# Performance work log

Hardware: AMD Instinct MI355X
Metric: run time of the kernel (lower is better)

The kernel has to match this reference:

```python
import jax, jax.numpy as jnp
import numpy as np

B, L, E, D = 4, 4096, 768, 64

def setup_inputs() -> dict:
    key = jax.random.key(0)
    ks = jax.random.split(key, 7)
    x = jax.random.normal(ks[0], (B, L, E), dtype=jnp.float32)
    # True = masked (strict upper triangle), as in masked_fill semantics
    causal_mask = jnp.triu(jnp.ones((L, L), dtype=bool), k=1)
    # True = valid token (inverted with ~ inside forward); all valid to avoid NaN rows
    pad_mask = jnp.ones((B, L), dtype=bool)
    s = 1.0 / np.sqrt(E)
    Wk = jax.random.uniform(ks[1], (E, D), jnp.float32, -s, s)
    bk = jax.random.uniform(ks[2], (D,), jnp.float32, -s, s)
    Wq = jax.random.uniform(ks[3], (E, D), jnp.float32, -s, s)
    bq = jax.random.uniform(ks[4], (D,), jnp.float32, -s, s)
    Wv = jax.random.uniform(ks[5], (E, D), jnp.float32, -s, s)
    bv = jax.random.uniform(ks[6], (D,), jnp.float32, -s, s)
    return {"x": x, "causal_mask": causal_mask, "pad_mask": pad_mask,
            "Wk": Wk, "bk": bk, "Wq": Wq, "bq": bq, "Wv": Wv, "bv": bv}

def reference(x, causal_mask, pad_mask, Wk, bk, Wq, bq, Wv, bv):
    # Linear projections: [B,L,E] @ [E,D] + [D]
    K = jnp.einsum('ble,ed->bld', x, Wk) + bk
    Q = jnp.einsum('ble,ed->bld', x, Wq) + bq
    V = jnp.einsum('ble,ed->bld', x, Wv) + bv
    d = Q.shape[-1]
    scores = jnp.einsum('bqd,bkd->bqk', Q, K) / jnp.sqrt(jnp.asarray(d, Q.dtype))
    # full_mask: causal (True=masked) OR key-position padding (~pad_mask, broadcast over query dim)
    full_mask = causal_mask[None, :, :] | (~pad_mask)[:, None, :]
    scores = jnp.where(full_mask, -jnp.inf, scores)
    attn = jax.nn.softmax(scores, axis=-1)
    out = jnp.einsum('bqk,bkd->bqd', attn, V)
    return out
```

## Files before the change

### kernel.cpp

```cpp
#include <hip/hip_runtime.h>

#define L_SEQ 4096
#define BATCH 4
#define EDIM 768

typedef __attribute__((ext_vector_type(8))) short bf16x8;
typedef __attribute__((ext_vector_type(4))) float f32x4;
typedef __attribute__((ext_vector_type(16))) float f32x16;
typedef __attribute__((ext_vector_type(4))) unsigned short u16x4;
typedef __attribute__((ext_vector_type(8))) unsigned short u16x8;
typedef __attribute__((ext_vector_type(2))) _Float16 f16x2;
typedef __attribute__((ext_vector_type(4))) _Float16 f16x4;

__device__ __forceinline__ unsigned short f2bf(float f) {
  unsigned u = __builtin_bit_cast(unsigned, f);
  u += 0x7FFFu + ((u >> 16) & 1u);
  return (unsigned short)(u >> 16);
}

__device__ __forceinline__ f16x4 half_of(u16x8 v, int h) {
  u16x4 t = h ? (u16x4){v[4], v[5], v[6], v[7]} : (u16x4){v[0], v[1], v[2], v[3]};
  return __builtin_bit_cast(f16x4, t);
}

__device__ __forceinline__ f16x2 pkrtz(float a, float b) {
  return __builtin_bit_cast(f16x2, __builtin_amdgcn_cvt_pkrtz(a, b));
}

__global__ __launch_bounds__(256) void prep_kernel(
    const float* __restrict__ Wq, const float* __restrict__ Wk,
    const float* __restrict__ Wv, unsigned short* __restrict__ WT) {
  int g = blockIdx.x * 256 + threadIdx.x;
  if (g >= 192 * EDIM) return;
  int row = g / EDIM, k = g - row * EDIM;
  int z = row >> 6, n = row & 63;
  const float* W = (z == 0) ? Wq : (z == 1) ? Wk : Wv;
  WT[g] = f2bf(W[k * 64 + n]);
}

__global__ __launch_bounds__(256) void proj_kernel(
    const float* __restrict__ x, const unsigned short* __restrict__ WT,
    const float* __restrict__ bq, const float* __restrict__ bk, const float* __restrict__ bv,
    unsigned short* __restrict__ Qf, unsigned short* __restrict__ Kf,
    unsigned short* __restrict__ Vf) {
  __shared__ unsigned short SH[2 * 13824];
  int tid = threadIdx.x;
  int w = tid >> 6, lane = tid & 63, l15 = lane & 15, g4 = lane >> 4;
  int m0 = blockIdx.x * 64;
  int brow = tid >> 3, bsg = tid & 7;

  f32x4 acc[3][4];
#pragma unroll
  for (int z = 0; z < 3; z++)
#pragma unroll
    for (int cf = 0; cf < 4; cf++) acc[z][cf] = (f32x4){0.f, 0.f, 0.f, 0.f};

  f32x4 arA[4], arB[4];
  u16x8 brA[6], brB[6];

  auto loadA = [&](f32x4 (&ar)[4], int k0) {
    const float* xp = x + (size_t)(m0 + 16 * w + l15) * EDIM + k0 + g4 * 8;
    ar[0] = *(const f32x4*)xp;
    ar[1] = *(const f32x4*)(xp + 4);
    ar[2] = *(const f32x4*)(xp + 32);
    ar[3] = *(const f32x4*)(xp + 36);
  };
  auto loadB = [&](u16x8 (&br)[6], int k0) {
#pragma unroll
    for (int pp = 0; pp < 6; pp++)
      br[pp] = *(const u16x8*)(WT + (size_t)(brow + pp * 32) * EDIM + k0 + bsg * 8);
  };
  auto writeB = [&](int cur, u16x8 (&br)[6]) {
#pragma unroll
    for (int pp = 0; pp < 6; pp++)
      *(u16x8*)&SH[cur * 13824 + (brow + pp * 32) * 72 + bsg * 8] = br[pp];
  };
  auto mkfrag = [&](f32x4 lo, f32x4 hi) {
    union { u16x8 u; bf16x8 b; } r;
    r.u[0] = f2bf(lo[0]); r.u[1] = f2bf(lo[1]); r.u[2] = f2bf(lo[2]); r.u[3] = f2bf(lo[3]);
    r.u[4] = f2bf(hi[0]); r.u[5] = f2bf(hi[1]); r.u[6] = f2bf(hi[2]); r.u[7] = f2bf(hi[3]);
    return r.b;
  };
  auto compute = [&](int cur, f32x4 (&ar)[4]) {
#pragma unroll
    for (int ks = 0; ks < 2; ks++) {
      bf16x8 a = mkfrag(ar[ks * 2], ar[ks * 2 + 1]);
#pragma unroll
      for (int z = 0; z < 3; z++)
#pragma unroll
        for (int cf = 0; cf < 4; cf++) {
          bf16x8 bb = *(const bf16x8*)&SH[cur * 13824 + (z * 64 + cf * 16 + l15) * 72 +
                                          ks * 32 + g4 * 8];
          acc[z][cf] = __builtin_amdgcn_mfma_f32_16x16x32_bf16(a, bb, acc[z][cf], 0, 0, 0);
        }
    }
  };

  loadA(arA, 0);
  loadB(brA, 0);
  for (int ss = 0; ss < 6; ss++) {
    int k1 = (2 * ss + 1) * 64;
    loadA(arB, k1);
    loadB(brB, k1);
    writeB(0, brA);
    __syncthreads();
    compute(0, arA);
    if (ss < 5) {
      int k2 = (2 * ss + 2) * 64;
      loadA(arA, k2);
      loadB(brA, k2);
    }
    writeB(1, brB);
    __syncthreads();
    compute(1, arB);
  }

  __syncthreads();
  unsigned short* LQ = SH;
  unsigned short* LK = SH + 4096;
  unsigned short* LV = SH + 8192;
#pragma unroll
  for (int cf = 0; cf < 4; cf++) {
    int d = cf * 16 + l15;
    float bqv = bq[d], bkv = bk[d], bvv = bv[d];
#pragma unroll
    for (int r = 0; r < 4; r++) {
      int t = 16 * w + g4 * 4 + r;
      int sl = t >> 5, tl = t & 31;
      int fqk = sl * 2048 + (d >> 4) * 512 + (tl + ((d >> 3) & 1) * 32) * 8 + (d & 7);
      LQ[fqk] = f2bf((acc[0][cf][r] + bqv) * 0.125f);
      LK[fqk] = f2bf(acc[1][cf][r] + bkv);
      int fv = sl * 2048 + (d >> 5) * 1024 + ((tl >> 4) & 1) * 512 +
               ((d & 31) + ((tl >> 2) & 1) * 32) * 8 + ((tl >> 3) & 1) * 4 + (tl & 3);
      _Float16 hv = (_Float16)(acc[2][cf][r] + bvv);
      LV[fv] = __builtin_bit_cast(unsigned short, hv);
    }
  }
  __syncthreads();
  {
    int bb = m0 >> 12;
    int S0 = (m0 >> 5) & 127;
    size_t base = ((size_t)(bb * 128 + S0)) * 2048;
    u16x8* dq = (u16x8*)(Qf + base);
    u16x8* dk = (u16x8*)(Kf + base);
    u16x8* dv = (u16x8*)(Vf + base);
    const u16x8* sq = (const u16x8*)LQ;
    const u16x8* sk = (const u16x8*)LK;
    const u16x8* sv = (const u16x8*)LV;
    dq[tid * 2] = sq[tid * 2]; dq[tid * 2 + 1] = sq[tid * 2 + 1];
    dk[tid * 2] = sk[tid * 2]; dk[tid * 2 + 1] = sk[tid * 2 + 1];
    dv[tid * 2] = sv[tid * 2]; dv[tid * 2 + 1] = sv[tid * 2 + 1];
  }
}

__global__ __launch_bounds__(512, 2) void attn_kernel(
    const unsigned short* __restrict__ Qf, const unsigned short* __restrict__ Kf,
    const unsigned short* __restrict__ Vf, float* __restrict__ out) {
  __shared__ float OB[8][32][68];
  __shared__ float ML[8][2][32];
  int tid = threadIdx.x;
  int w = tid >> 6, lane = tid & 63;
  int ql = lane & 31, hi = lane >> 5;
  int blk = blockIdx.x;
  int xcd = blk & 7;
  int b = xcd >> 1;
  int pid = ((xcd & 1) << 5) | (blk >> 3);
  int sA = pid, sB = 127 - pid;
  size_t bL = (size_t)b * L_SEQ;
  const unsigned short* Qb = Qf + (size_t)b * 128 * 2048;
  const unsigned short* Kb = Kf + (size_t)b * 128 * 2048;
  const unsigned short* Vb = Vf + (size_t)b * 128 * 2048;

  bf16x8 qA[4], qB[4];
#pragma unroll
  for (int kh = 0; kh < 4; kh++) {
    qA[kh] = *(const bf16x8*)(Qb + ((size_t)sA * 4 + kh) * 512 + lane * 8);
    qB[kh] = *(const bf16x8*)(Qb + ((size_t)sB * 4 + kh) * 512 + lane * 8);
  }
  f32x16 oA0, oA1, oB0, oB1;
#pragma unroll
  for (int i = 0; i < 16; i++) { oA0[i] = 0.f; oA1[i] = 0.f; oB0[i] = 0.f; oB1[i] = 0.f; }
  float mA = -1e38f, lA = 0.f, mB = -1e38f, lB = 0.f;

  auto loadKV = [&](bf16x8 (&kf)[4], u16x8 (&vf)[4], int j) {
    const unsigned short* kp = Kb + (size_t)j * 2048 + lane * 8;
    const unsigned short* vp = Vb + (size_t)j * 2048 + lane * 8;
#pragma unroll
    for (int q = 0; q < 4; q++) kf[q] = *(const bf16x8*)(kp + q * 512);
#pragma unroll
    for (int q = 0; q < 4; q++) vf[q] = *(const u16x8*)(vp + q * 512);
  };

  auto strip = [&](bf16x8 (&kf)[4], u16x8 (&vf)[4], int j, int s, bf16x8 (&qf)[4],
                   f32x16& o0, f32x16& o1, float& m, float& l) {
    f32x16 st;
#pragma unroll
    for (int i = 0; i < 16; i++) st[i] = 0.f;
    __builtin_amdgcn_s_setprio(1);
#pragma unroll
    for (int kh = 0; kh < 4; kh++)
      st = __builtin_amdgcn_mfma_f32_32x32x16_bf16(kf[kh], qf[kh], st, 0, 0, 0);
    __builtin_amdgcn_s_setprio(0);

    if (j == s) {
#pragma unroll
      for (int r = 0; r < 16; r++) {
        int tl = (r & 3) + 8 * (r >> 2) + 4 * hi;
        if (tl > ql) st[r] = -1e30f;
      }
    }

    float mx = st[0];
#pragma unroll
    for (int r = 1; r < 16; r++) mx = fmaxf(mx, st[r]);
    mx = fmaxf(mx, __shfl_xor(mx, 32));
    if (!__all(mx <= m + 8.0f)) {
      float mn = fmaxf(m, mx);
      float sc = __expf(m - mn);
      m = mn; l *= sc;
#pragma unroll
      for (int i = 0; i < 16; i++) { o0[i] *= sc; o1[i] *= sc; }
    }
    float rs = 0.f;
#pragma unroll
    for (int r = 0; r < 16; r++) { st[r] = __expf(st[r] - m); rs += st[r]; }
    rs += __shfl_xor(rs, 32);
    l += rs;

    f16x4 pb[4];
#pragma unroll
    for (int oc = 0; oc < 4; oc++) {
      f16x2 a = pkrtz(st[4 * oc], st[4 * oc + 1]);
      f16x2 c = pkrtz(st[4 * oc + 2], st[4 * oc + 3]);
      pb[oc] = (f16x4){a[0], a[1], c[0], c[1]};
    }
    __builtin_amdgcn_s_setprio(1);
#pragma unroll
    for (int oc = 0; oc < 4; oc++)
      o0 = __builtin_amdgcn_mfma_f32_32x32x8f16(half_of(vf[oc >> 1], oc & 1), pb[oc], o0, 0, 0, 0);
#pragma unroll
    for (int oc = 0; oc < 4; oc++)
      o1 = __builtin_amdgcn_mfma_f32_32x32x8f16(half_of(vf[2 + (oc >> 1)], oc & 1), pb[oc], o1, 0, 0, 0);
    __builtin_amdgcn_s_setprio(0);
  };

  auto step = [&](bf16x8 (&kf)[4], u16x8 (&vf)[4], int j) {
    if (j <= sA) strip(kf, vf, j, sA, qA, oA0, oA1, mA, lA);
    strip(kf, vf, j, sB, qB, oB0, oB1, mB, lB);
  };

  bf16x8 kfA[4], kfB[4];
  u16x8 vfA[4], vfB[4];
  {
    int j = w;
    loadKV(kfA, vfA, j);
    while (true) {
      int jn = j + 8;
      bool hasB = (jn <= sB);
      if (hasB) loadKV(kfB, vfB, jn);
      step(kfA, vfA, j);
      if (!hasB) break;
      j = jn;
      jn = j + 8;
      bool hasA = (jn <= sB);
      if (hasA) loadKV(kfA, vfA, jn);
      step(kfB, vfB, j);
      if (!hasA) break;
      j = jn;
    }
  }

  auto stash_reduce = [&](int s, f32x16& o0, f32x16& o1, float m, float l) {
    __syncthreads();
#pragma unroll
    for (int g = 0; g < 4; g++) {
      *(f32x4*)&OB[w][ql][8 * g + 4 * hi] =
          (f32x4){o0[4 * g], o0[4 * g + 1], o0[4 * g + 2], o0[4 * g + 3]};
      *(f32x4*)&OB[w][ql][32 + 8 * g + 4 * hi] =
          (f32x4){o1[4 * g], o1[4 * g + 1], o1[4 * g + 2], o1[4 * g + 3]};
    }
    if (hi == 0) { ML[w][0][ql] = m; ML[w][1][ql] = l; }
    __syncthreads();
    int q = tid >> 4, dg = tid & 15;
    float mw[8], lw[8];
    float ms = -1e38f;
#pragma unroll
    for (int ww = 0; ww < 8; ww++) {
      mw[ww] = ML[ww][0][q]; lw[ww] = ML[ww][1][q];
      ms = fmaxf(ms, mw[ww]);
    }
    float denom = 0.f, ew[8];
#pragma unroll
    for (int ww = 0; ww < 8; ww++) { ew[ww] = __expf(mw[ww] - ms); denom += lw[ww] * ew[ww]; }
    float inv = 1.0f / denom;
    f32x4 acc = (f32x4){0.f, 0.f, 0.f, 0.f};
#pragma unroll
    for (int ww = 0; ww < 8; ww++) {
      f32x4 v = *(const f32x4*)&OB[ww][q][dg * 4];
      acc += v * ew[ww];
    }
    acc *= inv;
    *(f32x4*)(out + (bL + (size_t)s * 32 + q) * 64 + dg * 4) = acc;
  };
  stash_reduce(sA, oA0, oA1, mA, lA);
  stash_reduce(sB, oB0, oB1, mB, lB);
}

extern "C" void kernel_launch(void* const* d_in, const int* in_sizes, int n_in,
                              void* d_out, int out_size, void* d_ws, size_t ws_size,
                              hipStream_t stream) {
  const float* x  = (const float*)d_in[0];
  const float* Wk = (const float*)d_in[3];
  const float* bk = (const float*)d_in[4];
  const float* Wq = (const float*)d_in[5];
  const float* bq = (const float*)d_in[6];
  const float* Wv = (const float*)d_in[7];
  const float* bv = (const float*)d_in[8];
  float* out = (float*)d_out;

  char* ws = (char*)d_ws;
  unsigned short* WT = (unsigned short*)ws;
  unsigned short* Qf = (unsigned short*)(ws + 294912);
  unsigned short* Kf = (unsigned short*)(ws + 294912 + 2097152);
  unsigned short* Vf = (unsigned short*)(ws + 294912 + 2 * 2097152);

  prep_kernel<<<576, 256, 0, stream>>>(Wq, Wk, Wv, WT);
  proj_kernel<<<256, 256, 0, stream>>>(x, WT, bq, bk, bv, Qf, Kf, Vf);
  attn_kernel<<<256, 512, 0, stream>>>(Qf, Kf, Vf, out);
}
```

Baseline: 48.13 us.

## Stage projection weights directly into LDS with pre-swizzled layout via global_load_lds

The weight-transpose prep kernel now writes the bf16 weights in a per-k-step tiled layout with an XOR swizzle. The projection kernel then copies each tile straight from global memory into LDS using global_load_lds, with no register round trip. The LDS tile drops its padding and the reads apply the matching XOR swizzle to avoid bank conflicts. The pipeline is reordered so each stage issues its loads before computing on the other buffer, which cuts VGPR pressure and copy instructions. This relies on correct ordering between the async LDS loads and the barriers.

```diff
diff --git a/kernel.cpp b/kernel.cpp
--- a/kernel.cpp
+++ b/kernel.cpp
@@ -27,27 +27,35 @@
   return __builtin_bit_cast(f16x2, __builtin_amdgcn_cvt_pkrtz(a, b));
 }
 
+__device__ __forceinline__ void gload_lds16(const void* g, void* l) {
+  __builtin_amdgcn_global_load_lds(
+      (const __attribute__((address_space(1))) void*)g,
+      (__attribute__((address_space(3))) void*)l, 16, 0, 0);
+}
+
 __global__ __launch_bounds__(256) void prep_kernel(
     const float* __restrict__ Wq, const float* __restrict__ Wk,
-    const float* __restrict__ Wv, unsigned short* __restrict__ WT) {
+    const float* __restrict__ Wv, unsigned short* __restrict__ WTT) {
   int g = blockIdx.x * 256 + threadIdx.x;
-  if (g >= 192 * EDIM) return;
-  int row = g / EDIM, k = g - row * EDIM;
+  int kstep = g / 12288, rem = g - kstep * 12288;
+  int row = rem >> 6, kc_lin = rem & 63;
   int z = row >> 6, n = row & 63;
+  int kc = kc_lin ^ ((row & 7) << 3);
+  int k = kstep * 64 + kc;
   const float* W = (z == 0) ? Wq : (z == 1) ? Wk : Wv;
-  WT[g] = f2bf(W[k * 64 + n]);
+  WTT[g] = f2bf(W[k * 64 + n]);
 }
 
 __global__ __launch_bounds__(256) void proj_kernel(
-    const float* __restrict__ x, const unsigned short* __restrict__ WT,
+    const float* __restrict__ x, const unsigned short* __restrict__ WTT,
     const float* __restrict__ bq, const float* __restrict__ bk, const float* __restrict__ bv,
     unsigned short* __restrict__ Qf, unsigned short* __restrict__ Kf,
     unsigned short* __restrict__ Vf) {
-  __shared__ unsigned short SH[2 * 13824];
+  __shared__ unsigned short SH[2 * 12288];
   int tid = threadIdx.x;
   int w = tid >> 6, lane = tid & 63, l15 = lane & 15, g4 = lane >> 4;
   int m0 = blockIdx.x * 64;
-  int brow = tid >> 3, bsg = tid & 7;
+  int sw = (l15 & 7) << 3;
 
   f32x4 acc[3][4];
 #pragma unroll
@@ -56,7 +64,6 @@
     for (int cf = 0; cf < 4; cf++) acc[z][cf] = (f32x4){0.f, 0.f, 0.f, 0.f};
 
   f32x4 arA[4], arB[4];
-  u16x8 brA[6], brB[6];
 
   auto loadA = [&](f32x4 (&ar)[4], int k0) {
     const float* xp = x + (size_t)(m0 + 16 * w + l15) * EDIM + k0 + g4 * 8;
@@ -65,15 +72,13 @@
     ar[2] = *(const f32x4*)(xp + 32);
     ar[3] = *(const f32x4*)(xp + 36);
   };
-  auto loadB = [&](u16x8 (&br)[6], int k0) {
-#pragma unroll
-    for (int pp = 0; pp < 6; pp++)
-      br[pp] = *(const u16x8*)(WT + (size_t)(brow + pp * 32) * EDIM + k0 + bsg * 8);
-  };
-  auto writeB = [&](int cur, u16x8 (&br)[6]) {
-#pragma unroll
-    for (int pp = 0; pp < 6; pp++)
-      *(u16x8*)&SH[cur * 13824 + (brow + pp * 32) * 72 + bsg * 8] = br[pp];
+  auto stageB = [&](int buf, int kstep) {
+    const unsigned short* src = WTT + (size_t)kstep * 12288;
+#pragma unroll
+    for (int i = 0; i < 6; i++) {
+      int c = i * 4 + w;
+      gload_lds16(src + c * 512 + lane * 8, &SH[buf * 12288 + c * 512]);
+    }
   };
   auto mkfrag = [&](f32x4 lo, f32x4 hi) {
     union { u16x8 u; bf16x8 b; } r;
@@ -89,33 +94,30 @@
       for (int z = 0; z < 3; z++)
 #pragma unroll
         for (int cf = 0; cf < 4; cf++) {
-          bf16x8 bb = *(const bf16x8*)&SH[cur * 13824 + (z * 64 + cf * 16 + l15) * 72 +
-                                          ks * 32 + g4 * 8];
+          bf16x8 bb = *(const bf16x8*)&SH[cur * 12288 + (z * 64 + cf * 16 + l15) * 64 +
+                                          ((ks * 32 + g4 * 8) ^ sw)];
           acc[z][cf] = __builtin_amdgcn_mfma_f32_16x16x32_bf16(a, bb, acc[z][cf], 0, 0, 0);
         }
     }
   };
 
+  stageB(0, 0);
   loadA(arA, 0);
-  loadB(brA, 0);
+  __syncthreads();
   for (int ss = 0; ss < 6; ss++) {
-    int k1 = (2 * ss + 1) * 64;
-    loadA(arB, k1);
-    loadB(brB, k1);
-    writeB(0, brA);
+    int t1 = 2 * ss + 1;
+    stageB(1, t1);
+    loadA(arB, t1 * 64);
+    compute(0, arA);
     __syncthreads();
-    compute(0, arA);
     if (ss < 5) {
-      int k2 = (2 * ss + 2) * 64;
-      loadA(arA, k2);
-      loadB(brA, k2);
-    }
-    writeB(1, brB);
+      stageB(0, t1 + 1);
+      loadA(arA, (t1 + 1) * 64);
+    }
+    compute(1, arB);
     __syncthreads();
-    compute(1, arB);
-  }
-
-  __syncthreads();
+  }
+
   unsigned short* LQ = SH;
   unsigned short* LK = SH + 4096;
   unsigned short* LV = SH + 8192;
@@ -138,18 +140,18 @@
   }
   __syncthreads();
   {
-    int bb = m0 >> 12;
+    int b_ = m0 >> 12;
     int S0 = (m0 >> 5) & 127;
-    size_t base = ((size_t)(bb * 128 + S0)) * 2048;
+    size_t base = ((size_t)(b_ * 128 + S0)) * 2048;
+    const u16x8* sq = (const u16x8*)LQ;
+    const u16x8* sk = (const u16x8*)LK;
+    const u16x8* sv = (const u16x8*)LV;
     u16x8* dq = (u16x8*)(Qf + base);
     u16x8* dk = (u16x8*)(Kf + base);
     u16x8* dv = (u16x8*)(Vf + base);
-    const u16x8* sq = (const u16x8*)LQ;
-    const u16x8* sk = (const u16x8*)LK;
-    const u16x8* sv = (const u16x8*)LV;
-    dq[tid * 2] = sq[tid * 2]; dq[tid * 2 + 1] = sq[tid * 2 + 1];
-    dk[tid * 2] = sk[tid * 2]; dk[tid * 2 + 1] = sk[tid * 2 + 1];
-    dv[tid * 2] = sv[tid * 2]; dv[tid * 2 + 1] = sv[tid * 2 + 1];
+    dq[tid] = sq[tid]; dq[tid + 256] = sq[tid + 256];
+    dk[tid] = sk[tid]; dk[tid + 256] = sk[tid + 256];
+    dv[tid] = sv[tid]; dv[tid + 256] = sv[tid + 256];
   }
 }
 
@@ -319,12 +321,12 @@
   float* out = (float*)d_out;
 
   char* ws = (char*)d_ws;
-  unsigned short* WT = (unsigned short*)ws;
-  unsigned short* Qf = (unsigned short*)(ws + 294912);
-  unsigned short* Kf = (unsigned short*)(ws + 294912 + 2097152);
-  unsigned short* Vf = (unsigned short*)(ws + 294912 + 2 * 2097152);
-
-  prep_kernel<<<576, 256, 0, stream>>>(Wq, Wk, Wv, WT);
-  proj_kernel<<<256, 256, 0, stream>>>(x, WT, bq, bk, bv, Qf, Kf, Vf);
+  unsigned short* WTT = (unsigned short*)ws;
+  unsigned short* Qf  = (unsigned short*)(ws + 294912);
+  unsigned short* Kf  = (unsigned short*)(ws + 294912 + 2097152);
+  unsigned short* Vf  = (unsigned short*)(ws + 294912 + 2 * 2097152);
+
+  prep_kernel<<<576, 256, 0, stream>>>(Wq, Wk, Wv, WTT);
+  proj_kernel<<<256, 256, 0, stream>>>(x, WTT, bq, bk, bv, Qf, Kf, Vf);
   attn_kernel<<<256, 512, 0, stream>>>(Qf, Kf, Vf, out);
 }
```

New measurement: 49.44 us. 1.03x slower.
